# Kernel tuning notes

Measured on AMD Instinct MI355X. Metric: run time of the kernel, lower is better.

Reference implementation:

```python
import jax, jax.numpy as jnp
import numpy as np

H = 16  # num_heads

def _rotate_half(x):
    x1, x2 = jnp.split(x, 2, axis=-1)
    return jnp.concatenate((-x2, x1), axis=-1)

def setup_inputs() -> dict:
    key = jax.random.key(0)
    ks = jax.random.split(key, 8)
    B, N, C = 4, 2048, 1024
    d = C // H
    x = jax.random.normal(ks[0], (B, N, C), dtype=jnp.float32)
    cos = jax.random.uniform(ks[1], (1, 1, N, d), dtype=jnp.float32)
    sin = jax.random.uniform(ks[2], (1, 1, N, d), dtype=jnp.float32)
    s = 0.02
    Wq = jax.random.normal(ks[3], (C, C), dtype=jnp.float32) * s
    Wkv = jax.random.normal(ks[4], (C, 2 * C), dtype=jnp.float32) * s
    Wout = jax.random.normal(ks[5], (C, C), dtype=jnp.float32) * s
    bout = jnp.zeros((C,), dtype=jnp.float32)
    return {"x": x, "cos": cos, "sin": sin, "Wq": Wq, "Wkv": Wkv, "Wout": Wout, "bout": bout}

def reference(x, cos, sin, Wq, Wkv, Wout, bout):
    B, N, C = x.shape
    d = C // H
    scale = d ** (-0.5)
    # projections (qkv_bias=False)
    q = (x @ Wq).reshape(B, N, H, d).transpose(0, 2, 1, 3)        # (B,H,N,d)
    kv = x @ Wkv                                                   # (B,N,2C)
    k, v = jnp.split(kv, 2, axis=-1)
    k = k.reshape(B, N, H, d).transpose(0, 2, 1, 3)
    v = v.reshape(B, N, H, d).transpose(0, 2, 1, 3)
    # inline RoPE
    q = q * cos + _rotate_half(q) * sin
    k = k * cos + _rotate_half(k) * sin
    # naive full attention
    sim = jnp.einsum('bhid,bhjd->bhij', q, k) * scale              # (B,H,N,N)
    attn = jax.nn.softmax(sim, axis=-1)
    out = jnp.einsum('bhij,bhjd->bhid', attn, v)                   # (B,H,N,d)
    out = out.transpose(0, 2, 1, 3).reshape(B, N, C)
    return out @ Wout + bout
```

## Files before the change

### kernel.cpp

```cpp
#include <hip/hip_runtime.h>


typedef unsigned short u16;
typedef unsigned int u32;
typedef __attribute__((ext_vector_type(4))) short s16x4;
typedef __attribute__((ext_vector_type(8))) short short8;
typedef __attribute__((ext_vector_type(8))) unsigned short ushort8;
typedef __attribute__((ext_vector_type(4))) float f32x4;

#define MFMA16x16x32 __builtin_amdgcn_mfma_f32_16x16x32_bf16
#define QSCALE 0.180336880434135f

#if __has_builtin(__builtin_amdgcn_exp2f)
#define EXP2F __builtin_amdgcn_exp2f
#else
#define EXP2F exp2f
#endif

__device__ __forceinline__ float b2f(u16 u) {
  union { u32 i; float f; } x; x.i = ((u32)u) << 16; return x.f;
}
__device__ __forceinline__ u16 f2b(float f) {
  union { float f; u32 i; } x; x.f = f;
  u32 r = (x.i + 0x7FFFu + ((x.i >> 16) & 1u)) >> 16;
  return (u16)r;
}
__device__ __forceinline__ u32 f2b_trunc32(float f) {
  union { float f; u32 i; } x; x.f = f;
  return x.i >> 16;
}
__device__ __forceinline__ bool detect_f32(const u32* __restrict__ cw) {
  u32 acc = 0;
#pragma unroll
  for (int i = 0; i < 64; ++i) acc |= cw[i];
  return (acc & 0x8000u) != 0;
}
__device__ __forceinline__ float ldval(const void* p, long i, bool f32) {
  return f32 ? ((const float*)p)[i] : b2f(((const u16*)p)[i]);
}
__device__ __forceinline__ ushort8 ld8f(const float* p) {
  float4 u0 = *(const float4*)p;
  float4 u1 = *(const float4*)(p + 4);
  ushort8 r;
  r[0] = f2b(u0.x); r[1] = f2b(u0.y); r[2] = f2b(u0.z); r[3] = f2b(u0.w);
  r[4] = f2b(u1.x); r[5] = f2b(u1.y); r[6] = f2b(u1.z); r[7] = f2b(u1.w);
  return r;
}
__device__ __forceinline__ void async16(const void* g, void* l) {
  __builtin_amdgcn_global_load_lds((const __attribute__((address_space(1))) void*)g,
                                   (__attribute__((address_space(3))) void*)l, 16, 0, 0);
}

__global__ __launch_bounds__(256)
void prep(const void* __restrict__ x, u16* __restrict__ x_bf16,
          const void* __restrict__ Wq, const void* __restrict__ Wkv,
          u16* __restrict__ WT1, const u32* __restrict__ cosw) {
  const bool f32 = detect_f32(cosw);
  const int b = blockIdx.x;
  const int t = threadIdx.x;
  if (b < 4096) {
    const long i = ((long)b * 256 + t) * 8;
    ushort8 v;
    if (f32) v = ld8f((const float*)x + i);
    else     v = *(const ushort8*)((const u16*)x + i);
    *(ushort8*)(x_bf16 + i) = v;
    return;
  }
  __shared__ __align__(16) u16 tile[64][65];
  const void* src; u16* dst; int R, C, bx, by;
  if (b < 4352) {
    const int idx = b - 4096;
    src = Wq;  dst = WT1;               R = 1024; C = 1024;
    bx = idx & 15; by = idx >> 4;
  } else {
    const int idx = b - 4352;
    src = Wkv; dst = WT1 + 1024 * 1024; R = 1024; C = 2048;
    bx = idx & 31; by = idx >> 5;
  }
  const int tr = by * 64, tc = bx * 64;
#pragma unroll
  for (int i = 0; i < 2; ++i) {
    const int ch = i * 256 + t;
    const int r = ch >> 3, cc = ch & 7;
    ushort8 v;
    if (f32) v = ld8f((const float*)src + (long)(tr + r) * C + tc + cc * 8);
    else     v = *(const ushort8*)((const u16*)src + (long)(tr + r) * C + tc + cc * 8);
#pragma unroll
    for (int j = 0; j < 8; ++j) tile[r][cc * 8 + j] = v[j];
  }
  __syncthreads();
#pragma unroll
  for (int i = 0; i < 2; ++i) {
    const int ch = i * 256 + t;
    const int c = ch >> 3, rc = ch & 7;
    ushort8 v;
#pragma unroll
    for (int j = 0; j < 8; ++j) v[j] = tile[rc * 8 + j][c];
    *(ushort8*)(dst + (long)(tc + c) * R + tr + rc * 8) = v;
  }
}

__global__ __launch_bounds__(256)
void transpose_any(const void* __restrict__ src, u16* __restrict__ dst,
                   int R, int C, const u32* __restrict__ cosw) {
  const bool f32 = detect_f32(cosw);
  const int tr = blockIdx.y * 64, tc = blockIdx.x * 64;
  __shared__ __align__(16) u16 tile[64][65];
  const int t = threadIdx.x;
#pragma unroll
  for (int i = 0; i < 2; ++i) {
    const int ch = i * 256 + t;
    const int r = ch >> 3, cc = ch & 7;
    ushort8 v;
    if (f32) v = ld8f((const float*)src + (long)(tr + r) * C + tc + cc * 8);
    else     v = *(const ushort8*)((const u16*)src + (long)(tr + r) * C + tc + cc * 8);
#pragma unroll
    for (int j = 0; j < 8; ++j) tile[r][cc * 8 + j] = v[j];
  }
  __syncthreads();
#pragma unroll
  for (int i = 0; i < 2; ++i) {
    const int ch = i * 256 + t;
    const int c = ch >> 3, rc = ch & 7;
    ushort8 v;
#pragma unroll
    for (int j = 0; j < 8; ++j) v[j] = tile[rc * 8 + j][c];
    *(ushort8*)(dst + (long)(tc + c) * R + tr + rc * 8) = v;
  }
}

template <int MODE>
__global__ __launch_bounds__(256)
void gemm_fast(const u16* __restrict__ A, const u16* __restrict__ BT,
               const void* cosp, const void* sinp,
               u16* q_ws, u16* k_ws, u16* vT_ws,
               const void* bias, void* outp, const u32* __restrict__ cosw) {
  constexpr int K = 1024, ITERS = K / 32;
  constexpr int NBX = (MODE == 0) ? 24 : 8;
  __shared__ __align__(16) u16 As[2][128 * 32];
  __shared__ __align__(16) u16 Bs[2][128 * 32];
  const int tid = threadIdx.x;
  const int wave = tid >> 6, lane = tid & 63;
  const int quad = lane >> 4, l15 = lane & 15;
  const int mh = (wave >> 1) * 64, nh = (wave & 1) * 64;
  const f32x4 zero4 = {0.f, 0.f, 0.f, 0.f};

  const int w = blockIdx.y * NBX + blockIdx.x;
  const int xcd = w & 7, idx = w >> 3;
  int bx, by;
  if (MODE == 0) {
    const int xc = idx / 48, r = idx % 48;
    by = xcd * 8 + r / 6;
    bx = xc * 6 + r % 6;
  } else {
    by = xcd * 8 + idx / 8;
    bx = idx % 8;
  }
  const int m0 = by * 128, n0 = bx * 128;

  f32x4 acc[4][4];
#pragma unroll
  for (int i = 0; i < 4; ++i)
#pragma unroll
    for (int j = 0; j < 4; ++j) acc[i][j] = zero4;

  const int c0 = tid, c1 = 256 + tid;
  const u16* a0p = A  + (long)(m0 + (c0 >> 2)) * K + (((c0 & 3) ^ ((c0 >> 3) & 3)) * 8);
  const u16* a1p = A  + (long)(m0 + (c1 >> 2)) * K + (((c1 & 3) ^ ((c1 >> 3) & 3)) * 8);
  const u16* b0p = BT + (long)(n0 + (c0 >> 2)) * K + (((c0 & 3) ^ ((c0 >> 3) & 3)) * 8);
  const u16* b1p = BT + (long)(n0 + (c1 >> 2)) * K + (((c1 & 3) ^ ((c1 >> 3) & 3)) * 8);

#define STAGE(buf, kt)                                \
  do {                                                \
    async16(a0p + (kt), As[buf] + c0 * 8);            \
    async16(a1p + (kt), As[buf] + c1 * 8);            \
    async16(b0p + (kt), Bs[buf] + c0 * 8);            \
    async16(b1p + (kt), Bs[buf] + c1 * 8);            \
  } while (0)

  const int rk = (quad ^ ((l15 >> 1) & 3)) * 8;

  STAGE(0, 0);
  for (int it = 0; it < ITERS; ++it) {
    const int cur = it & 1;
    __syncthreads();
    if (it + 1 < ITERS) STAGE(cur ^ 1, (it + 1) * 32);
    short8 af[4], bf[4];
#pragma unroll
    for (int s = 0; s < 4; ++s) {
      af[s] = *(const short8*)(As[cur] + (mh + s * 16 + l15) * 32 + rk);
      bf[s] = *(const short8*)(Bs[cur] + (nh + s * 16 + l15) * 32 + rk);
    }
#pragma unroll
    for (int i = 0; i < 4; ++i)
#pragma unroll
      for (int j = 0; j < 4; ++j)
        acc[i][j] = MFMA16x16x32(af[i], bf[j], acc[i][j], 0, 0, 0);
  }
#undef STAGE

  const bool f32 = detect_f32(cosw);

  if (MODE == 0) {
    const int seg = n0 >> 10;
    const int csbase = (n0 & 1023) + nh;
    if (seg == 2) {
#pragma unroll
      for (int i = 0; i < 4; ++i) {
        const int mm0 = m0 + mh + i * 16 + quad * 4;
        const int b = mm0 >> 11, nb = mm0 & 2047;
#pragma unroll
        for (int j = 0; j < 4; ++j) {
          const int cs = csbase + j * 16 + l15;
          const int h = cs >> 6, dv = cs & 63;
          s16x4 pk4;
#pragma unroll
          for (int r = 0; r < 4; ++r) pk4[r] = (short)f2b(acc[i][j][r]);
          *(s16x4*)(vT_ws + (((long)((b * 16 + h) * 64 + dv)) << 11) + nb) = pk4;
        }
      }
    } else {
      u16* segp = (seg == 0) ? q_ws : k_ws;
#pragma unroll
      for (int i = 0; i < 4; ++i) {
#pragma unroll
        for (int r = 0; r < 4; ++r) {
          const int mm = m0 + mh + i * 16 + quad * 4 + r;
          const int b = mm >> 11, n = mm & 2047;
#pragma unroll
          for (int j = 0; j < 4; ++j) {
            const int cs = csbase + j * 16 + l15;
            const int h = cs >> 6, dv = cs & 63;
            const float cv = ldval(cosp, (long)n * 64 + dv, f32);
            const float sv = ldval(sinp, (long)n * 64 + dv, f32);
            const float part = acc[i][j ^ 2][r];
            float val = acc[i][j][r] * cv + ((dv < 32) ? -part : part) * sv;
            if (seg == 0) val *= QSCALE;
            segp[(((long)(b * 16 + h) * 2048 + n) << 6) + dv] = f2b(val);
          }
        }
      }
    }
  } else {
#pragma unroll
    for (int i = 0; i < 4; ++i) {
#pragma unroll
      for (int r = 0; r < 4; ++r) {
        const int mm = m0 + mh + i * 16 + quad * 4 + r;
#pragma unroll
        for (int j = 0; j < 4; ++j) {
          const int cc = n0 + nh + j * 16 + l15;
          const float val = acc[i][j][r] + ldval(bias, cc, f32);
          if (f32) ((float*)outp)[(long)mm * 1024 + cc] = val;
          else     ((u16*)outp)[(long)mm * 1024 + cc] = f2b(val);
        }
      }
    }
  }
}

__global__ __launch_bounds__(512, 4)
void flash_k(const u16* __restrict__ q_ws, const u16* __restrict__ k_ws,
             const u16* __restrict__ vT_ws, u16* __restrict__ attn) {
  __shared__ __align__(16) u16 Ks[2][128 * 64];
  __shared__ __align__(16) u16 Vts[2][64 * 128];
  const int tid = threadIdx.x, wave = tid >> 6, lane = tid & 63;
  const int quad = lane >> 4, l15 = lane & 15;
  const int s7 = l15 & 7;
  const int bid = blockIdx.x + (blockIdx.y << 3);
  const int qx = bid >> 6;
  const int bh = ((bid & 7) << 3) | ((bid >> 3) & 7);
  const int qr0 = qx * 256 + wave * 32;
  const u16* Q  = q_ws  + (long)bh * 2048 * 64;
  const u16* Kp = k_ws  + (long)bh * 2048 * 64;
  const u16* Vt = vT_ws + (long)bh * 64 * 2048;
  const f32x4 zero4 = {0.f, 0.f, 0.f, 0.f};
  short8 ones;
#pragma unroll
  for (int i = 0; i < 8; ++i) ones[i] = (short)0x3F80;

  short8 aq[2][2];
#pragma unroll
  for (int ms = 0; ms < 2; ++ms)
#pragma unroll
    for (int ks = 0; ks < 2; ++ks)
      aq[ms][ks] = *(const short8*)(Q + (long)(qr0 + ms * 16 + l15) * 64 + ks * 32 + quad * 8);

  f32x4 accO[2][4], accL[2];
#pragma unroll
  for (int ms = 0; ms < 2; ++ms) {
#pragma unroll
    for (int jd = 0; jd < 4; ++jd) accO[ms][jd] = zero4;
    accL[ms] = zero4;
  }

  const int kc0 = tid, kc1 = 512 + tid;
  const int kr0 = kc0 >> 3, kg0 = ((kc0 & 7) ^ (kr0 & 7)) * 8;
  const int kr1 = kc1 >> 3, kg1 = ((kc1 & 7) ^ (kr1 & 7)) * 8;
  const int vr0 = kc0 >> 4, vg0 = ((kc0 & 15) ^ (vr0 & 7)) * 8;
  const int vr1 = kc1 >> 4, vg1 = ((kc1 & 15) ^ (vr1 & 7)) * 8;

#define STAGEKV(buf, kt)                                             \
  do {                                                               \
    async16(Kp + (long)((kt) + kr0) * 64 + kg0, Ks[buf] + kc0 * 8);  \
    async16(Kp + (long)((kt) + kr1) * 64 + kg1, Ks[buf] + kc1 * 8);  \
    async16(Vt + (long)vr0 * 2048 + (kt) + vg0, Vts[buf] + kc0 * 8); \
    async16(Vt + (long)vr1 * 2048 + (kt) + vg1, Vts[buf] + kc1 * 8); \
  } while (0)

  const int vh = (quad & 1) * 4;
  const int qh = quad >> 1;

  STAGEKV(0, 0);
  for (int it = 0; it < 16; ++it) {
    const int cur = it & 1;
    __syncthreads();
    if (it + 1 < 16) STAGEKV(cur ^ 1, (it + 1) * 128);

#pragma unroll
    for (int k2 = 0; k2 < 4; ++k2) {
      u32 pk[2][4];
#pragma unroll
      for (int nsl = 0; nsl < 2; ++nsl) {
        const int ns = k2 * 2 + nsl;
        const u16* rowK = Ks[cur] + (ns * 16 + l15) * 64;
        short8 b0 = *(const short8*)(rowK + ((quad ^ s7) * 8));
        short8 b1 = *(const short8*)(rowK + (((quad + 4) ^ s7) * 8));
#pragma unroll
        for (int ms = 0; ms < 2; ++ms) {
          f32x4 t = MFMA16x16x32(b0, aq[ms][0], zero4, 0, 0, 0);
          f32x4 sa = MFMA16x16x32(b1, aq[ms][1], t, 0, 0, 0);
          const u32 p0 = f2b_trunc32(EXP2F(sa[0]));
          const u32 p1 = f2b_trunc32(EXP2F(sa[1]));
          const u32 p2 = f2b_trunc32(EXP2F(sa[2]));
          const u32 p3 = f2b_trunc32(EXP2F(sa[3]));
          pk[ms][nsl * 2 + 0] = p0 | (p1 << 16);
          pk[ms][nsl * 2 + 1] = p2 | (p3 << 16);
        }
      }
      __builtin_amdgcn_s_setprio(1);
      short8 ap[2];
#pragma unroll
      for (int ms = 0; ms < 2; ++ms) {
        union { u32 w[4]; short8 s; } u;
        u.w[0] = pk[ms][0]; u.w[1] = pk[ms][1];
        u.w[2] = pk[ms][2]; u.w[3] = pk[ms][3];
        ap[ms] = u.s;
        accL[ms] = MFMA16x16x32(ap[ms], ones, accL[ms], 0, 0, 0);
      }
      const int ca = ((4 * k2 + qh) ^ s7) * 8 + vh;
      const int cb = ((4 * k2 + 2 + qh) ^ s7) * 8 + vh;
#pragma unroll
      for (int jd = 0; jd < 4; ++jd) {
        const u16* rowV = Vts[cur] + (jd * 16 + l15) * 128;
        union { s16x4 h[2]; short8 s; } bv;
        bv.h[0] = *(const s16x4*)(rowV + ca);
        bv.h[1] = *(const s16x4*)(rowV + cb);
#pragma unroll
        for (int ms = 0; ms < 2; ++ms)
          accO[ms][jd] = MFMA16x16x32(ap[ms], bv.s, accO[ms][jd], 0, 0, 0);
      }
      __builtin_amdgcn_s_setprio(0);
    }
  }
#undef STAGEKV

  const int b = bh >> 4, h = bh & 15;
#pragma unroll
  for (int ms = 0; ms < 2; ++ms) {
#pragma unroll
    for (int r = 0; r < 4; ++r) {
      const float inv = 1.f / accL[ms][r];
      const int row = qr0 + ms * 16 + quad * 4 + r;
#pragma unroll
      for (int jd = 0; jd < 4; ++jd) {
        const int cc = h * 64 + jd * 16 + l15;
        attn[((long)(b * 2048 + row)) * 1024 + cc] = f2b(accO[ms][jd][r] * inv);
      }
    }
  }
}

extern "C" void kernel_launch(void* const* d_in, const int* in_sizes, int n_in,
                              void* d_out, int out_size, void* d_ws, size_t ws_size,
                              hipStream_t stream) {
  const void* x    = d_in[0];
  const void* cosp = d_in[1];
  const void* sinp = d_in[2];
  const void* Wq   = d_in[3];
  const void* Wkv  = d_in[4];
  const void* Wout = d_in[5];
  const void* bout = d_in[6];
  const u32* cosw  = (const u32*)d_in[1];

  char* ws = (char*)d_ws;
  const size_t MB = 1u << 20;
  u16* q_ws  = (u16*)(ws);
  u16* k_ws  = (u16*)(ws + 16 * MB);
  u16* vT_ws = (u16*)(ws + 32 * MB);
  u16* attn  = (u16*)(ws + 48 * MB);
  u16* WoutT = (u16*)(ws + 32 * MB);

  u16* WT1;
  if (ws_size >= 88 * MB) WT1 = (u16*)(ws + 64 * MB);
  else                    WT1 = (u16*)d_out;
  u16* x_bf16 = WT1 + 3072 * 1024;

  prep<<<dim3(4864), 256, 0, stream>>>(x, x_bf16, Wq, Wkv, WT1, cosw);
  gemm_fast<0><<<dim3(24, 64), 256, 0, stream>>>(x_bf16, WT1, cosp, sinp,
                                                 q_ws, k_ws, vT_ws,
                                                 nullptr, nullptr, cosw);
  flash_k<<<dim3(8, 64), 512, 0, stream>>>(q_ws, k_ws, vT_ws, attn);
  transpose_any<<<dim3(16, 16), 256, 0, stream>>>(Wout, WoutT, 1024, 1024, cosw);
  gemm_fast<1><<<dim3(8, 64), 256, 0, stream>>>(attn, WoutT, cosp, sinp,
                                                nullptr, nullptr, nullptr,
                                                bout, d_out, cosw);
}
```

Before: 298.2 us.

## Use 256x128 tiles with XCD-aware block swizzle for QKV projection GEMM

Adds a dedicated QKV projection kernel whose block tile is 256x128 instead of 128x128, with each wave holding an 8x4 accumulator grid. A and B fragments are therefore reused over twice as many MFMAs, and there are half as many blocks. Block indices are remapped so that groups of neighbouring tiles land on the same XCD, which is meant to improve L2 reuse of A and B panels. The cost is much higher register pressure (128 accumulator floats per lane) and more LDS, which may lower occupancy or cause spills. The RoPE and layout epilogue is unchanged apart from the new tile indexing.

```diff
diff --git a/kernel.cpp b/kernel.cpp
--- a/kernel.cpp
+++ b/kernel.cpp
@@ -126,6 +126,112 @@
 #pragma unroll
     for (int j = 0; j < 8; ++j) v[j] = tile[rc * 8 + j][c];
     *(ushort8*)(dst + (long)(tc + c) * R + tr + rc * 8) = v;
+  }
+}
+
+__global__ __launch_bounds__(256, 2)
+void gemm_qkv(const u16* __restrict__ A, const u16* __restrict__ BT,
+              const void* cosp, const void* sinp,
+              u16* q_ws, u16* k_ws, u16* vT_ws,
+              const u32* __restrict__ cosw) {
+  constexpr int K = 1024, ITERS = K / 32;
+  __shared__ __align__(16) u16 As[2][256 * 32];
+  __shared__ __align__(16) u16 Bs[2][128 * 32];
+  const int tid = threadIdx.x;
+  const int wave = tid >> 6, lane = tid & 63;
+  const int quad = lane >> 4, l15 = lane & 15;
+  const int wr = wave >> 1, wc = wave & 1;
+  const f32x4 zero4 = {0.f, 0.f, 0.f, 0.f};
+
+  const int w = blockIdx.y * 24 + blockIdx.x;
+  const int xcd = w & 7, idx = w >> 3;
+  const int xc = idx / 24, rr = idx % 24;
+  const int by = xcd * 4 + rr / 6;
+  const int bx = xc * 6 + rr % 6;
+  const int m0 = by * 256, n0 = bx * 128;
+
+  f32x4 acc[8][4];
+#pragma unroll
+  for (int i = 0; i < 8; ++i)
+#pragma unroll
+    for (int j = 0; j < 4; ++j) acc[i][j] = zero4;
+
+  const int srow = tid >> 2;
+  const int ks8 = ((tid & 3) ^ ((tid >> 3) & 3)) * 8;
+  const u16* ap = A  + (long)(m0 + srow) * K + ks8;
+  const u16* bp = BT + (long)(n0 + srow) * K + ks8;
+
+#define STAGEQ(buf, kt)                                                   \
+  do {                                                                    \
+    _Pragma("unroll")                                                     \
+    for (int p = 0; p < 4; ++p)                                           \
+      async16(ap + (long)(p * 64) * K + (kt), As[buf] + (p * 256 + tid) * 8); \
+    _Pragma("unroll")                                                     \
+    for (int p = 0; p < 2; ++p)                                           \
+      async16(bp + (long)(p * 64) * K + (kt), Bs[buf] + (p * 256 + tid) * 8); \
+  } while (0)
+
+  const int rk = (quad ^ ((l15 >> 1) & 3)) * 8;
+
+  STAGEQ(0, 0);
+  for (int it = 0; it < ITERS; ++it) {
+    const int cur = it & 1;
+    __syncthreads();
+    if (it + 1 < ITERS) STAGEQ(cur ^ 1, (it + 1) * 32);
+    short8 af[8], bf[4];
+#pragma unroll
+    for (int s = 0; s < 8; ++s)
+      af[s] = *(const short8*)(As[cur] + (wr * 128 + s * 16 + l15) * 32 + rk);
+#pragma unroll
+    for (int j = 0; j < 4; ++j)
+      bf[j] = *(const short8*)(Bs[cur] + (wc * 64 + j * 16 + l15) * 32 + rk);
+#pragma unroll
+    for (int i = 0; i < 8; ++i)
+#pragma unroll
+      for (int j = 0; j < 4; ++j)
+        acc[i][j] = MFMA16x16x32(af[i], bf[j], acc[i][j], 0, 0, 0);
+  }
+#undef STAGEQ
+
+  const bool f32 = detect_f32(cosw);
+  const int seg = n0 >> 10;
+  const int csbase = (n0 & 1023) + wc * 64;
+  if (seg == 2) {
+#pragma unroll
+    for (int i = 0; i < 8; ++i) {
+      const int mm0 = m0 + wr * 128 + i * 16 + quad * 4;
+      const int b = mm0 >> 11, nb = mm0 & 2047;
+#pragma unroll
+      for (int j = 0; j < 4; ++j) {
+        const int cs = csbase + j * 16 + l15;
+        const int h = cs >> 6, dv = cs & 63;
+        s16x4 pk4;
+#pragma unroll
+        for (int r = 0; r < 4; ++r) pk4[r] = (short)f2b(acc[i][j][r]);
+        *(s16x4*)(vT_ws + (((long)((b * 16 + h) * 64 + dv)) << 11) + nb) = pk4;
+      }
+    }
+  } else {
+    u16* segp = (seg == 0) ? q_ws : k_ws;
+#pragma unroll
+    for (int i = 0; i < 8; ++i) {
+#pragma unroll
+      for (int r = 0; r < 4; ++r) {
+        const int mm = m0 + wr * 128 + i * 16 + quad * 4 + r;
+        const int b = mm >> 11, n = mm & 2047;
+#pragma unroll
+        for (int j = 0; j < 4; ++j) {
+          const int cs = csbase + j * 16 + l15;
+          const int h = cs >> 6, dv = cs & 63;
+          const float cv = ldval(cosp, (long)n * 64 + dv, f32);
+          const float sv = ldval(sinp, (long)n * 64 + dv, f32);
+          const float part = acc[i][j ^ 2][r];
+          float val = acc[i][j][r] * cv + ((dv < 32) ? -part : part) * sv;
+          if (seg == 0) val *= QSCALE;
+          segp[(((long)(b * 16 + h) * 2048 + n) << 6) + dv] = f2b(val);
+        }
+      }
+    }
   }
 }
 
@@ -201,47 +307,7 @@
 
   const bool f32 = detect_f32(cosw);
 
-  if (MODE == 0) {
-    const int seg = n0 >> 10;
-    const int csbase = (n0 & 1023) + nh;
-    if (seg == 2) {
-#pragma unroll
-      for (int i = 0; i < 4; ++i) {
-        const int mm0 = m0 + mh + i * 16 + quad * 4;
-        const int b = mm0 >> 11, nb = mm0 & 2047;
-#pragma unroll
-        for (int j = 0; j < 4; ++j) {
-          const int cs = csbase + j * 16 + l15;
-          const int h = cs >> 6, dv = cs & 63;
-          s16x4 pk4;
-#pragma unroll
-          for (int r = 0; r < 4; ++r) pk4[r] = (short)f2b(acc[i][j][r]);
-          *(s16x4*)(vT_ws + (((long)((b * 16 + h) * 64 + dv)) << 11) + nb) = pk4;
-        }
-      }
-    } else {
-      u16* segp = (seg == 0) ? q_ws : k_ws;
-#pragma unroll
-      for (int i = 0; i < 4; ++i) {
-#pragma unroll
-        for (int r = 0; r < 4; ++r) {
-          const int mm = m0 + mh + i * 16 + quad * 4 + r;
-          const int b = mm >> 11, n = mm & 2047;
-#pragma unroll
-          for (int j = 0; j < 4; ++j) {
-            const int cs = csbase + j * 16 + l15;
-            const int h = cs >> 6, dv = cs & 63;
-            const float cv = ldval(cosp, (long)n * 64 + dv, f32);
-            const float sv = ldval(sinp, (long)n * 64 + dv, f32);
-            const float part = acc[i][j ^ 2][r];
-            float val = acc[i][j][r] * cv + ((dv < 32) ? -part : part) * sv;
-            if (seg == 0) val *= QSCALE;
-            segp[(((long)(b * 16 + h) * 2048 + n) << 6) + dv] = f2b(val);
-          }
-        }
-      }
-    }
-  } else {
+  if (MODE == 1) {
 #pragma unroll
     for (int i = 0; i < 4; ++i) {
 #pragma unroll
@@ -407,9 +473,8 @@
   u16* x_bf16 = WT1 + 3072 * 1024;
 
   prep<<<dim3(4864), 256, 0, stream>>>(x, x_bf16, Wq, Wkv, WT1, cosw);
-  gemm_fast<0><<<dim3(24, 64), 256, 0, stream>>>(x_bf16, WT1, cosp, sinp,
-                                                 q_ws, k_ws, vT_ws,
-                                                 nullptr, nullptr, cosw);
+  gemm_qkv<<<dim3(24, 32), 256, 0, stream>>>(x_bf16, WT1, cosp, sinp,
+                                             q_ws, k_ws, vT_ws, cosw);
   flash_k<<<dim3(8, 64), 512, 0, stream>>>(q_ws, k_ws, vT_ws, attn);
   transpose_any<<<dim3(16, 16), 256, 0, stream>>>(Wout, WoutT, 1024, 1024, cosw);
   gemm_fast<1><<<dim3(8, 64), 256, 0, stream>>>(attn, WoutT, cosp, sinp,
```

After: 290.8 us. -2.5%, faster.
